# Performance work log

Hardware: AMD Instinct MI355X
Metric: run time of the kernel (lower is better)

Reference implementation:

```python
import jax, jax.numpy as jnp
import numpy as np

B, T, C, L = 256, 512, 128, 64  # batch, timesteps, num_classes (blank=C-1), max label len
NEG = -1e30  # finite -inf surrogate (avoids nan in grads)


def setup_inputs() -> dict:
    key = jax.random.key(0)
    k1, k2, k3, k4 = jax.random.split(key, 4)
    logits = jax.random.normal(k1, (B, T, C), dtype=jnp.float32)
    y_pred = jax.nn.softmax(logits, axis=-1)  # ctc_batch_cost expects softmax probs
    y_true = jax.random.randint(k2, (B, L), 0, C - 1, dtype=jnp.int32)  # non-blank labels
    input_length = jax.random.randint(k3, (B, 1), T // 2, T + 1, dtype=jnp.int32)
    label_length = jax.random.randint(k4, (B, 1), L // 2, L + 1, dtype=jnp.int32)
    return {"y_true": y_true, "y_pred": y_pred,
            "input_length": input_length, "label_length": label_length}


def _ctc_loss(log_probs, labels, input_length, label_length, blank):
    # log_probs: [B,T,C]; labels: [B,L]; lengths: [B]
    b, t_max, _ = log_probs.shape
    l_max = labels.shape[1]
    s_max = 2 * l_max + 1
    # extended label sequence: blank, l1, blank, l2, ..., blank  -> [B,S]
    ext = jnp.full((b, s_max), blank, dtype=labels.dtype)
    ext = ext.at[:, 1::2].set(labels)
    # gathered log probs per extended symbol: [B,T,S]
    lp = jnp.take_along_axis(log_probs, ext[:, None, :].astype(jnp.int32), axis=2)
    # skip (s-2 -> s) allowed where ext[s] != blank and ext[s] != ext[s-2]
    skip = jnp.zeros((b, s_max), dtype=bool)
    skip = skip.at[:, 2:].set((ext[:, 2:] != blank) & (ext[:, 2:] != ext[:, :-2]))
    # init alpha at t=0: only s=0 (blank) and s=1 (first label) reachable
    alpha0 = jnp.full((b, s_max), NEG, dtype=log_probs.dtype)
    alpha0 = alpha0.at[:, 0].set(lp[:, 0, 0])
    alpha0 = alpha0.at[:, 1].set(lp[:, 0, 1])
    in_len = input_length

    def step(alpha, inp):
        lp_t, t = inp  # lp_t: [B,S]
        s1 = jnp.pad(alpha, ((0, 0), (1, 0)), constant_values=NEG)[:, :-1]
        s2 = jnp.pad(alpha, ((0, 0), (2, 0)), constant_values=NEG)[:, :-2]
        a = jnp.logaddexp(alpha, s1)
        a = jnp.where(skip, jnp.logaddexp(a, s2), a)
        new = a + lp_t
        new = jnp.where((t < in_len)[:, None], new, alpha)  # freeze past input_length
        return new, None

    lp_time_major = jnp.swapaxes(lp, 0, 1)  # [T,B,S]
    ts = jnp.arange(1, t_max)
    alpha, _ = jax.lax.scan(step, alpha0, (lp_time_major[1:], ts))
    lab = label_length
    idx_last = 2 * lab  # final blank position; idx_last-1 is final label position
    a_last = jnp.take_along_axis(alpha, idx_last[:, None], axis=1)[:, 0]
    a_prev = jnp.take_along_axis(alpha, (idx_last - 1)[:, None], axis=1)[:, 0]
    return -jnp.logaddexp(a_last, a_prev)  # [B]


def reference(y_true, y_pred, input_length, label_length):
    eps = 1e-7  # keras epsilon added before log
    log_probs = jnp.log(y_pred + eps)
    blank = y_pred.shape[-1] - 1  # keras ctc_batch_cost blank convention
    loss = _ctc_loss(log_probs, y_true, input_length[:, 0], label_length[:, 0], blank)
    return loss[:, None]  # [B,1], matching tf expand_dims(ctc_loss, 1)
```

## Files before the change

### kernel.cpp

```cpp
#include <hip/hip_runtime.h>


#define B_ 256
#define T_ 512
#define C_ 128
#define L_ 64
#define BLANK_ 127
#define EPSF (1e-7f)
#define CHUNK 32
#define LN2F 0.6931471805599453f

#define EXP2(x) __builtin_amdgcn_exp2f(x)
#define LOG2(x) __builtin_amdgcn_logf(x)

__device__ __forceinline__ float lse2_2(float a, float b) {
    float m = fmaxf(a, b);
    float d = fminf(a, b) - m;
    return m + LOG2(1.0f + EXP2(d));
}

__device__ __forceinline__ float dppf(float x) {
    return __int_as_float(__builtin_amdgcn_update_dpp(
        0, __float_as_int(x), 0x138, 0xf, 0xf, false));
}
__device__ __forceinline__ int dppi(int x) {
    return __builtin_amdgcn_update_dpp(0, x, 0x138, 0xf, 0xf, false);
}

__device__ __forceinline__ float delta_scale(int ep, int e) {
    int d = ep - e;
    d = d < -126 ? -126 : d;
    d = d > 126 ? 126 : d;
    return __int_as_float((d + 127) << 23);
}

__device__ __forceinline__ void renorm3(float& A0, float& A1, float& A2, int& e) {
    float m = fmaxf(fmaxf(A0, A1), A2);
    const int mb = __float_as_int(m);
    const bool valid = (unsigned)(mb - 0x00800000) < 0x7f000000u;
    int ex = (mb >> 23) - 127;
    ex = valid ? ex : 0;
    const float s = __int_as_float((127 - ex) << 23);
    A0 *= s; A1 *= s; A2 *= s;
    e += ex;
}

__device__ __forceinline__ void stage_chunk(const float* gsrc, float* ldst, int lane) {
#pragma unroll
    for (int i = 0; i < CHUNK / 2; ++i) {
        __builtin_amdgcn_global_load_lds(
            (const __attribute__((address_space(1))) void*)(gsrc + i * 256 + lane * 4),
            (__attribute__((address_space(3))) void*)(ldst + i * 256),
            16, 0, 0);
    }
}

struct Probs { float pl[16]; float pb[16]; };

__device__ __forceinline__ void loadA(const float* __restrict__ Lb, int base,
                                      int label, float pbv, Probs& P) {
#pragma unroll
    for (int u = 0; u < 16; ++u)
        P.pl[u] = Lb[(base + u) * C_ + label];
#pragma unroll
    for (int u = 0; u < 16; ++u)
        P.pb[u] = __int_as_float(
            __builtin_amdgcn_readlane(__float_as_int(pbv), base + u));
}

__device__ __forceinline__ void finishA(Probs& P) {
#pragma unroll
    for (int u = 0; u < 16; ++u) {
        P.pl[u] += EPSF;
        asm volatile("" : "+v"(P.pl[u]));
    }
}

template<bool FULL>
__device__ __forceinline__ void fat_group(const Probs& P, int lo, int hi,
    float skipf, float& A0, float& A1, float& A2, int& e)
{
#pragma unroll
    for (int u = 0; u < 16; ++u) {
        const float p1 = dppf(A1);
        const int   ep = dppi(e);
        const bool dead = (fmaxf(A0, A1) == 0.0f);
        const int   e1 = dead ? ep : e;
        const float sc = delta_scale(ep, e1);
        const float P1 = p1 * sc;
        const float A0o = A0, A1o = A1;
        const float nA0 = (A0o + P1) * P.pb[u];
        const float t   = fmaf(skipf, P1, A0o);
        const float nA1 = (A1o + t) * P.pl[u];
        const float nA2 = (A2 + A1o) * P.pb[u];
        if (FULL) { A0 = nA0; A1 = nA1; A2 = nA2; e = e1; }
        else {
            const bool v = (u >= lo) & (u < hi);
            A0 = v ? nA0 : A0o; A1 = v ? nA1 : A1o;
            A2 = v ? nA2 : A2;  e  = v ? e1 : e;
        }
        if ((u & 3) == 3) renorm3(A0, A1, A2, e);
    }
}

template<bool GUARD>
__device__ __forceinline__ void lean_group(const Probs& P, int hi, float skipf,
    float& A0, float& A1, float& A2, int& e, float& sc)
{
#pragma unroll
    for (int u = 0; u < 16; ++u) {
        const float P1 = dppf(A1) * sc;
        const float A0o = A0, A1o = A1;
        const float nA0 = (A0o + P1) * P.pb[u];
        const float t   = fmaf(skipf, P1, A0o);
        const float nA1 = (A1o + t) * P.pl[u];
        const float nA2 = (A2 + A1o) * P.pb[u];
        if (GUARD) {
            const bool v = u < hi;
            A0 = v ? nA0 : A0o; A1 = v ? nA1 : A1o; A2 = v ? nA2 : A2;
        } else { A0 = nA0; A1 = nA1; A2 = nA2; }
        if ((u & 3) == 3) {
            renorm3(A0, A1, A2, e);
            sc = delta_scale(dppi(e), e);
        }
    }
}

__global__ __launch_bounds__(64) void ctc_fwd_kernel(
    const int* __restrict__ y_true, const float* __restrict__ y_pred,
    const int* __restrict__ input_len, const int* __restrict__ label_len,
    float* __restrict__ out)
{
    __shared__ float lds[2][CHUNK * C_];
    const int b = blockIdx.x;
    const int lane = threadIdx.x;
    const float* __restrict__ P = y_pred + (size_t)b * T_ * C_;

    const int label = y_true[b * L_ + lane];
    const int lprev = __shfl_up(label, 1);
    const float skipf = (lane > 0 && label != lprev) ? 1.0f : 0.0f;

    const int in_len = input_len[b];
    const int lab    = label_len[b];
    const int tend = in_len < T_ ? in_len : T_;
    const int nchunks = (tend + CHUNK - 1) / CHUNK;

    stage_chunk(P, &lds[0][0], lane);
    stage_chunk(P + CHUNK * C_, &lds[1][0], lane);

    float A0 = 0.0f, A1 = 0.0f, A2 = 0.0f, sc = 1.0f;
    int e = 0;

    for (int c = 0; c < nchunks; ++c) {
        if (c + 1 < nchunks) asm volatile("s_waitcnt vmcnt(16)" ::: "memory");
        else                 asm volatile("s_waitcnt vmcnt(0)" ::: "memory");
        const float* __restrict__ Lb = lds[c & 1];
        const float pbv = Lb[(lane & 31) * C_ + BLANK_] + EPSF;

        Probs Pg0, Pg1;
        loadA(Lb, 0, label, pbv, Pg0);
        __builtin_amdgcn_sched_barrier(0);
        finishA(Pg0);
        loadA(Lb, 16, label, pbv, Pg1);
        __builtin_amdgcn_sched_barrier(0);

        if (c == 0) {
            A0 = (lane == 0) ? Lb[BLANK_] + EPSF : 0.0f;
            A1 = (lane == 0) ? Lb[label]  + EPSF : 0.0f;
            fat_group<false>(Pg0, 1, 16, skipf, A0, A1, A2, e);
            finishA(Pg1);
            fat_group<true >(Pg1, 0, 0, skipf, A0, A1, A2, e);
        } else if (c < 4) {
            fat_group<true>(Pg0, 0, 0, skipf, A0, A1, A2, e);
            finishA(Pg1);
            fat_group<true>(Pg1, 0, 0, skipf, A0, A1, A2, e);
        } else {
            if (c == 4) sc = delta_scale(dppi(e), e);
            const int rem = tend - c * CHUNK;
            if (rem >= CHUNK) {
                lean_group<false>(Pg0, 16, skipf, A0, A1, A2, e, sc);
                finishA(Pg1);
                lean_group<false>(Pg1, 16, skipf, A0, A1, A2, e, sc);
            } else if (rem > 16) {
                lean_group<false>(Pg0, 16, skipf, A0, A1, A2, e, sc);
                finishA(Pg1);
                lean_group<true >(Pg1, rem - 16, skipf, A0, A1, A2, e, sc);
            } else {
                lean_group<true>(Pg0, rem, skipf, A0, A1, A2, e, sc);
            }
        }
        if (c + 2 < nchunks)
            stage_chunk(P + (size_t)(c + 2) * CHUNK * C_, &lds[c & 1][0], lane);
    }

    const float ef = (float)e;
    const float l0 = LOG2(A0) + ef;
    const float l1 = LOG2(A1) + ef;
    const float l2 = LOG2(A2) + ef;
    const float a_prev = __shfl(l1, lab - 1);
    const float a_last = (lab >= L_) ? __shfl(l2, 63)
                                     : __shfl(l0, lab);
    if (lane == 0) out[b] = -LN2F * lse2_2(a_last, a_prev);
}

extern "C" void kernel_launch(void* const* d_in, const int* in_sizes, int n_in,
                              void* d_out, int out_size, void* d_ws, size_t ws_size,
                              hipStream_t stream) {
    const int*   y_true    = (const int*)d_in[0];
    const float* y_pred    = (const float*)d_in[1];
    const int*   input_len = (const int*)d_in[2];
    const int*   label_len = (const int*)d_in[3];
    float* out = (float*)d_out;

    ctc_fwd_kernel<<<B_, 64, 0, stream>>>(y_true, y_pred, input_len, label_len, out);
}
```

Baseline: 28.95 us.

## Split CTC kernel into producer and consumer wavefronts with blank-normalized probabilities

```diff
diff --git a/kernel.cpp b/kernel.cpp
--- a/kernel.cpp
+++ b/kernel.cpp
@@ -8,6 +8,7 @@
 #define BLANK_ 127
 #define EPSF (1e-7f)
 #define CHUNK 32
+#define QSTR 36
 #define LN2F 0.6931471805599453f
 
 #define EXP2(x) __builtin_amdgcn_exp2f(x)
@@ -34,12 +35,9 @@
     return __int_as_float((d + 127) << 23);
 }
 
-__device__ __forceinline__ void renorm3(float& A0, float& A1, float& A2, int& e) {
-    float m = fmaxf(fmaxf(A0, A1), A2);
-    const int mb = __float_as_int(m);
-    const bool valid = (unsigned)(mb - 0x00800000) < 0x7f000000u;
-    int ex = (mb >> 23) - 127;
-    ex = valid ? ex : 0;
+__device__ __forceinline__ void renorm(float& A0, float& A1, float& A2, int& e) {
+    const float m = fmaxf(fmaxf(A0, A1), A2);
+    const int ex = (__float_as_int(m) >> 23) - 127;
     const float s = __int_as_float((127 - ex) << 23);
     A0 *= s; A1 *= s; A2 *= s;
     e += ex;
@@ -55,152 +53,190 @@
     }
 }
 
-struct Probs { float pl[16]; float pb[16]; };
-
-__device__ __forceinline__ void loadA(const float* __restrict__ Lb, int base,
-                                      int label, float pbv, Probs& P) {
-#pragma unroll
-    for (int u = 0; u < 16; ++u)
-        P.pl[u] = Lb[(base + u) * C_ + label];
-#pragma unroll
-    for (int u = 0; u < 16; ++u)
-        P.pb[u] = __int_as_float(
-            __builtin_amdgcn_readlane(__float_as_int(pbv), base + u));
-}
-
-__device__ __forceinline__ void finishA(Probs& P) {
-#pragma unroll
-    for (int u = 0; u < 16; ++u) {
-        P.pl[u] += EPSF;
-        asm volatile("" : "+v"(P.pl[u]));
+__device__ __forceinline__ void produce_chunk(const float* __restrict__ rk,
+        float* __restrict__ qd, int lane, int label, int t0, int tend, float& llg)
+{
+    const float pbv  = rk[(lane & 31) * C_ + BLANK_] + EPSF;
+    const float rpb  = 1.0f / pbv;
+    const float erpb = EPSF * rpb;
+    const int t = t0 + lane;
+    const bool lgv = (lane < 32) && (t >= 1) && (t < tend);
+    llg += lgv ? LOG2(pbv) : 0.0f;
+#pragma unroll
+    for (int r = 0; r < CHUNK; ++r) {
+        const float pl = rk[r * C_ + label];
+        const float rb = __int_as_float(
+            __builtin_amdgcn_readlane(__float_as_int(rpb), r));
+        const float eb = __int_as_float(
+            __builtin_amdgcn_readlane(__float_as_int(erpb), r));
+        qd[lane * QSTR + r] = fmaf(pl, rb, eb);
     }
 }
 
-template<bool FULL>
-__device__ __forceinline__ void fat_group(const Probs& P, int lo, int hi,
-    float skipf, float& A0, float& A1, float& A2, int& e)
-{
-#pragma unroll
-    for (int u = 0; u < 16; ++u) {
-        const float p1 = dppf(A1);
-        const int   ep = dppi(e);
-        const bool dead = (fmaxf(A0, A1) == 0.0f);
-        const int   e1 = dead ? ep : e;
-        const float sc = delta_scale(ep, e1);
-        const float P1 = p1 * sc;
-        const float A0o = A0, A1o = A1;
-        const float nA0 = (A0o + P1) * P.pb[u];
-        const float t   = fmaf(skipf, P1, A0o);
-        const float nA1 = (A1o + t) * P.pl[u];
-        const float nA2 = (A2 + A1o) * P.pb[u];
-        if (FULL) { A0 = nA0; A1 = nA1; A2 = nA2; e = e1; }
-        else {
-            const bool v = (u >= lo) & (u < hi);
-            A0 = v ? nA0 : A0o; A1 = v ? nA1 : A1o;
-            A2 = v ? nA2 : A2;  e  = v ? e1 : e;
-        }
-        if ((u & 3) == 3) renorm3(A0, A1, A2, e);
-    }
-}
-
-template<bool GUARD>
-__device__ __forceinline__ void lean_group(const Probs& P, int hi, float skipf,
-    float& A0, float& A1, float& A2, int& e, float& sc)
-{
-#pragma unroll
-    for (int u = 0; u < 16; ++u) {
-        const float P1 = dppf(A1) * sc;
-        const float A0o = A0, A1o = A1;
-        const float nA0 = (A0o + P1) * P.pb[u];
-        const float t   = fmaf(skipf, P1, A0o);
-        const float nA1 = (A1o + t) * P.pl[u];
-        const float nA2 = (A2 + A1o) * P.pb[u];
-        if (GUARD) {
-            const bool v = u < hi;
-            A0 = v ? nA0 : A0o; A1 = v ? nA1 : A1o; A2 = v ? nA2 : A2;
-        } else { A0 = nA0; A1 = nA1; A2 = nA2; }
-        if ((u & 3) == 3) {
-            renorm3(A0, A1, A2, e);
-            sc = delta_scale(dppi(e), e);
-        }
-    }
-}
-
-__global__ __launch_bounds__(64) void ctc_fwd_kernel(
+__device__ __forceinline__ void fat_step(float& A0, float& A1, float& A2, int& e,
+                                         float skipf, float ql) {
+    const float p1 = dppf(A1);
+    const int   ep = dppi(e);
+    const bool dead = (A0 + A1) == 0.0f;
+    const int   e1 = dead ? ep : e;
+    const float P1 = p1 * delta_scale(ep, e1);
+    const float A0o = A0, A1o = A1;
+    A0 = A0o + P1;
+    const float t = fmaf(skipf, P1, A0o);
+    A1 = (A1o + t) * ql;
+    A2 = A2 + A1o;
+    e  = e1;
+}
+
+__device__ __forceinline__ void lean_step(float& A0, float& A1, float& A2,
+                                          float sc, float skipf, float ql) {
+    const float P1 = dppf(A1) * sc;
+    const float A0o = A0, A1o = A1;
+    A0 = A0o + P1;
+    const float t = fmaf(skipf, P1, A0o);
+    A1 = (A1o + t) * ql;
+    A2 = A2 + A1o;
+}
+
+__global__ __launch_bounds__(128) void ctc_fwd_kernel(
     const int* __restrict__ y_true, const float* __restrict__ y_pred,
     const int* __restrict__ input_len, const int* __restrict__ label_len,
     float* __restrict__ out)
 {
-    __shared__ float lds[2][CHUNK * C_];
+    __shared__ __align__(16) float raw[2][CHUNK * C_];
+    __shared__ __align__(16) float qlbuf[2][64 * QSTR];
+    __shared__ float extra[4];
+
     const int b = blockIdx.x;
-    const int lane = threadIdx.x;
-    const float* __restrict__ P = y_pred + (size_t)b * T_ * C_;
-
+    const int tid = threadIdx.x;
+    const int lane = tid & 63;
+    const float* __restrict__ Pg = y_pred + (size_t)b * T_ * C_;
     const int label = y_true[b * L_ + lane];
-    const int lprev = __shfl_up(label, 1);
-    const float skipf = (lane > 0 && label != lprev) ? 1.0f : 0.0f;
-
     const int in_len = input_len[b];
-    const int lab    = label_len[b];
     const int tend = in_len < T_ ? in_len : T_;
-    const int nchunks = (tend + CHUNK - 1) / CHUNK;
-
-    stage_chunk(P, &lds[0][0], lane);
-    stage_chunk(P + CHUNK * C_, &lds[1][0], lane);
-
-    float A0 = 0.0f, A1 = 0.0f, A2 = 0.0f, sc = 1.0f;
-    int e = 0;
-
-    for (int c = 0; c < nchunks; ++c) {
-        if (c + 1 < nchunks) asm volatile("s_waitcnt vmcnt(16)" ::: "memory");
-        else                 asm volatile("s_waitcnt vmcnt(0)" ::: "memory");
-        const float* __restrict__ Lb = lds[c & 1];
-        const float pbv = Lb[(lane & 31) * C_ + BLANK_] + EPSF;
-
-        Probs Pg0, Pg1;
-        loadA(Lb, 0, label, pbv, Pg0);
-        __builtin_amdgcn_sched_barrier(0);
-        finishA(Pg0);
-        loadA(Lb, 16, label, pbv, Pg1);
-        __builtin_amdgcn_sched_barrier(0);
-
-        if (c == 0) {
-            A0 = (lane == 0) ? Lb[BLANK_] + EPSF : 0.0f;
-            A1 = (lane == 0) ? Lb[label]  + EPSF : 0.0f;
-            fat_group<false>(Pg0, 1, 16, skipf, A0, A1, A2, e);
-            finishA(Pg1);
-            fat_group<true >(Pg1, 0, 0, skipf, A0, A1, A2, e);
-        } else if (c < 4) {
-            fat_group<true>(Pg0, 0, 0, skipf, A0, A1, A2, e);
-            finishA(Pg1);
-            fat_group<true>(Pg1, 0, 0, skipf, A0, A1, A2, e);
-        } else {
-            if (c == 4) sc = delta_scale(dppi(e), e);
+    const int nmax = (tend + CHUNK - 1) / CHUNK;
+
+    if (tid >= 64) {
+        float llg = 0.0f;
+        stage_chunk(Pg, &raw[0][0], lane);
+        stage_chunk(Pg + CHUNK * C_, &raw[1][0], lane);
+        asm volatile("s_waitcnt vmcnt(16)" ::: "memory");
+        produce_chunk(&raw[0][0], &qlbuf[0][0], lane, label, 0, tend, llg);
+        if (lane == 0) {
+            extra[0] = raw[0][label] + EPSF;
+            extra[1] = raw[0][BLANK_] + EPSF;
+        }
+        asm volatile("s_waitcnt lgkmcnt(0)" ::: "memory");
+        __builtin_amdgcn_s_barrier();
+        for (int c = 0; c < nmax; ++c) {
+            if (c + 2 < nmax)
+                stage_chunk(Pg + (size_t)(c + 2) * CHUNK * C_, &raw[c & 1][0], lane);
+            if (c + 1 < nmax) {
+                if (c + 2 < nmax) asm volatile("s_waitcnt vmcnt(16)" ::: "memory");
+                else              asm volatile("s_waitcnt vmcnt(0)" ::: "memory");
+                produce_chunk(&raw[(c + 1) & 1][0], &qlbuf[(c + 1) & 1][0],
+                              lane, label, (c + 1) * CHUNK, tend, llg);
+            }
+            asm volatile("s_waitcnt lgkmcnt(0)" ::: "memory");
+            __builtin_amdgcn_s_barrier();
+        }
+#pragma unroll
+        for (int off = 16; off >= 1; off >>= 1) llg += __shfl_xor(llg, off);
+        if (lane == 0) extra[2] = llg;
+        asm volatile("s_waitcnt lgkmcnt(0)" ::: "memory");
+        __builtin_amdgcn_s_barrier();
+    } else {
+        const int lprev = __shfl_up(label, 1);
+        const float skipf = (lane > 0 && label != lprev) ? 1.0f : 0.0f;
+        const int lab = label_len[b];
+        __builtin_amdgcn_s_barrier();
+
+        float A0 = (lane == 0) ? extra[1] : 0.0f;
+        float A1 = (lane == 0) ? extra[0] : 0.0f;
+        float A2 = 0.0f, sc = 1.0f;
+        int e = 0;
+
+        {
+            const float* qb = &qlbuf[0][lane * QSTR];
+            float qlv[32];
+#pragma unroll
+            for (int k = 0; k < 8; ++k) {
+                const float4 t4 = *reinterpret_cast<const float4*>(qb + 4 * k);
+                qlv[4*k+0] = t4.x; qlv[4*k+1] = t4.y;
+                qlv[4*k+2] = t4.z; qlv[4*k+3] = t4.w;
+            }
+            __builtin_amdgcn_sched_barrier(0);
+#pragma unroll
+            for (int u = 1; u < 32; ++u) {
+                fat_step(A0, A1, A2, e, skipf, qlv[u]);
+                if ((u & 3) == 3) renorm(A0, A1, A2, e);
+            }
+            __builtin_amdgcn_s_barrier();
+        }
+        for (int c = 1; c < 4; ++c) {
+            const float* qb = &qlbuf[c & 1][lane * QSTR];
+            float qlv[32];
+#pragma unroll
+            for (int k = 0; k < 8; ++k) {
+                const float4 t4 = *reinterpret_cast<const float4*>(qb + 4 * k);
+                qlv[4*k+0] = t4.x; qlv[4*k+1] = t4.y;
+                qlv[4*k+2] = t4.z; qlv[4*k+3] = t4.w;
+            }
+            __builtin_amdgcn_sched_barrier(0);
+#pragma unroll
+            for (int u = 0; u < 32; ++u) {
+                fat_step(A0, A1, A2, e, skipf, qlv[u]);
+                if ((u & 3) == 3) renorm(A0, A1, A2, e);
+            }
+            __builtin_amdgcn_s_barrier();
+        }
+        sc = delta_scale(dppi(e), e);
+        for (int c = 4; c < nmax; ++c) {
+            const float* qb = &qlbuf[c & 1][lane * QSTR];
+            float qlv[32];
+#pragma unroll
+            for (int k = 0; k < 8; ++k) {
+                const float4 t4 = *reinterpret_cast<const float4*>(qb + 4 * k);
+                qlv[4*k+0] = t4.x; qlv[4*k+1] = t4.y;
+                qlv[4*k+2] = t4.z; qlv[4*k+3] = t4.w;
+            }
+            __builtin_amdgcn_sched_barrier(0);
             const int rem = tend - c * CHUNK;
             if (rem >= CHUNK) {
-                lean_group<false>(Pg0, 16, skipf, A0, A1, A2, e, sc);
-                finishA(Pg1);
-                lean_group<false>(Pg1, 16, skipf, A0, A1, A2, e, sc);
-            } else if (rem > 16) {
-                lean_group<false>(Pg0, 16, skipf, A0, A1, A2, e, sc);
-                finishA(Pg1);
-                lean_group<true >(Pg1, rem - 16, skipf, A0, A1, A2, e, sc);
+#pragma unroll
+                for (int u = 0; u < 32; ++u) {
+                    lean_step(A0, A1, A2, sc, skipf, qlv[u]);
+                    if ((u & 3) == 3) {
+                        renorm(A0, A1, A2, e);
+                        sc = delta_scale(dppi(e), e);
+                    }
+                }
             } else {
-                lean_group<true>(Pg0, rem, skipf, A0, A1, A2, e, sc);
-            }
-        }
-        if (c + 2 < nchunks)
-            stage_chunk(P + (size_t)(c + 2) * CHUNK * C_, &lds[c & 1][0], lane);
+#pragma unroll
+                for (int u = 0; u < 32; ++u) {
+                    const float A0o = A0, A1o = A1, A2o = A2;
+                    lean_step(A0, A1, A2, sc, skipf, qlv[u]);
+                    const bool v = u < rem;
+                    A0 = v ? A0 : A0o; A1 = v ? A1 : A1o; A2 = v ? A2 : A2o;
+                    if ((u & 3) == 3) {
+                        renorm(A0, A1, A2, e);
+                        sc = delta_scale(dppi(e), e);
+                    }
+                }
+            }
+            __builtin_amdgcn_s_barrier();
+        }
+        __builtin_amdgcn_s_barrier();
+        const float lg = extra[2];
+        const float ef = (float)e + lg;
+        const float l0 = LOG2(A0) + ef;
+        const float l1 = LOG2(A1) + ef;
+        const float l2 = LOG2(A2) + ef;
+        const float a_prev = __shfl(l1, lab - 1);
+        const float a_last = (lab >= L_) ? __shfl(l2, 63)
+                                         : __shfl(l0, lab);
+        if (lane == 0) out[b] = -LN2F * lse2_2(a_last, a_prev);
     }
-
-    const float ef = (float)e;
-    const float l0 = LOG2(A0) + ef;
-    const float l1 = LOG2(A1) + ef;
-    const float l2 = LOG2(A2) + ef;
-    const float a_prev = __shfl(l1, lab - 1);
-    const float a_last = (lab >= L_) ? __shfl(l2, 63)
-                                     : __shfl(l0, lab);
-    if (lane == 0) out[b] = -LN2F * lse2_2(a_last, a_prev);
 }
 
 extern "C" void kernel_launch(void* const* d_in, const int* in_sizes, int n_in,
@@ -212,5 +248,5 @@
     const int*   label_len = (const int*)d_in[3];
     float* out = (float*)d_out;
 
-    ctc_fwd_kernel<<<B_, 64, 0, stream>>>(y_true, y_pred, input_len, label_len, out);
-}
+    ctc_fwd_kernel<<<B_, 128, 0, stream>>>(y_true, y_pred, input_len, label_len, out);
+}
```

Result: faster. 26.07 us (-10.0%).
